# Optimization experiments

Hardware: AMD Instinct MI355X
Metric: run time of the kernel (lower is better)

Reference implementation:

```python
import jax, jax.numpy as jnp
import numpy as np

N_NODES = 50000
N_EDGES = 800000
IN_F = 128
OUT_F = 32
HEADS = 4
EDGE_DIM = 8
ALPHA = 0.2  # LeakyReLU negative slope


def setup_inputs() -> dict:
    key = jax.random.key(0)
    k0, k1, k2, k3, k4 = jax.random.split(key, 5)
    x = jax.random.normal(k0, (N_NODES, IN_F), dtype=jnp.float32)
    edge_index = jax.random.randint(k1, (2, N_EDGES), 0, N_NODES, dtype=jnp.int32)
    edge_attr = jax.random.normal(k2, (N_EDGES, EDGE_DIM), dtype=jnp.float32)
    # xavier-ish init for parameters
    W = jax.random.normal(k3, (HEADS, IN_F, OUT_F), dtype=jnp.float32) * (1.0 / np.float32(np.sqrt(IN_F)))
    a = jax.random.normal(k4, (HEADS, 2 * OUT_F + EDGE_DIM, 1), dtype=jnp.float32) * np.float32(0.1)
    return {"x": x, "edge_index": edge_index, "edge_attr": edge_attr, "W": W, "a": a}


def reference(x, edge_index, edge_attr, W, a):
    n_nodes = x.shape[0]
    out_f = W.shape[2]
    src, dst = edge_index[0], edge_index[1]

    # per-head linear transform: (N, H, O)
    xt = jnp.einsum('ni,hio->nho', x, W)
    x_src = xt[src]  # (E, H, O) edge gather
    x_dst = xt[dst]  # (E, H, O)

    # split attention vector a = [a_src | a_dst | a_edge]; equivalent to
    # einsum('ehi,hio->eho', cat([x_src, x_dst, edge]), a) without the concat
    av = a[..., 0]                      # (H, 2O+D)
    a_s = av[:, :out_f]                 # (H, O)
    a_d = av[:, out_f:2 * out_f]        # (H, O)
    a_e = av[:, 2 * out_f:]             # (H, D)
    e = (jnp.einsum('eho,ho->eh', x_src, a_s)
         + jnp.einsum('eho,ho->eh', x_dst, a_d)
         + edge_attr @ a_e.T)           # (E, H)
    e = jnp.where(e > 0, e, ALPHA * e)  # LeakyReLU

    # segment (per-destination) softmax over incoming edges, per head
    max_e = jax.ops.segment_max(e, dst, num_segments=n_nodes)   # (N, H), -inf on empty
    max_e = jnp.where(jnp.isneginf(max_e), jnp.zeros_like(max_e), max_e)
    exp_e = jnp.exp(e - max_e[dst])                             # (E, H)
    sum_exp = jax.ops.segment_sum(exp_e, dst, num_segments=n_nodes)  # (N, H)
    attention = exp_e / (sum_exp[dst] + 1e-10)                  # (E, H)

    # weighted scatter-add aggregation
    weighted = x_src * attention[:, :, None]                    # (E, H, O)
    out = jax.ops.segment_sum(weighted, dst, num_segments=n_nodes)  # (N, H, O)
    return out.reshape(n_nodes, -1)  # concat=True -> (N, H*O)
```

## Files before the change

### kernel.cpp

```cpp
#include <hip/hip_runtime.h>
#include <hip/hip_fp16.h>

#define N_NODES 50000
#define N_EDGES 800000
#define IN_F    128
#define OUT_F   32
#define HEADS   4
#define EDGE_DIM 8
#define LRELU_ALPHA 0.2f

#define EPB 2048
#define BT  1024
#define EPT (EPB / BT)
#define NBUCK 98
#define NBLK_A ((N_EDGES + EPB - 1) / EPB)
#define NODES_PER_BUCK 512
#define CAP 10240

typedef float    floatx4 __attribute__((ext_vector_type(4)));
typedef unsigned uintx4  __attribute__((ext_vector_type(4)));
typedef short    short4v __attribute__((ext_vector_type(4)));
typedef short    short8v __attribute__((ext_vector_type(8)));
typedef float    f32x4   __attribute__((ext_vector_type(4)));

__device__ __forceinline__ unsigned f2bf(float f) {
  unsigned u = __float_as_uint(f);
  return (u + 0x7fffu + ((u >> 16) & 1u)) >> 16;
}

__global__ __launch_bounds__(128) void k_wprep(
    const float* __restrict__ W, unsigned short* __restrict__ wtg,
    unsigned* __restrict__ bfill) {
  const int row = blockIdx.x;
  const int i = threadIdx.x;
  if (row == 0 && i < NBUCK) bfill[i] = (unsigned)(i * CAP);
  const float v = W[(row >> 5) * (IN_F * OUT_F) + i * OUT_F + (row & 31)];
  wtg[row * 128 + i] = (unsigned short)f2bf(v);
}

__global__ __launch_bounds__(256) void k_transform(
    const float* __restrict__ x, const unsigned short* __restrict__ wtg,
    unsigned* __restrict__ xtb) {
  __shared__ short sxb[64][136];
  const int t = threadIdx.x;
  const int n0 = blockIdx.x * 64;

#pragma unroll
  for (int r = 0; r < 8; ++r) {
    const int f = r * 256 + t;
    const int node = f >> 5;
    const int i4 = (f & 31) * 4;
    const int n = n0 + node;
    float4 v = make_float4(0.f, 0.f, 0.f, 0.f);
    if (n < N_NODES) v = *reinterpret_cast<const float4*>(&x[(size_t)n * 128 + i4]);
    short4v s4;
    s4.x = (short)f2bf(v.x);
    s4.y = (short)f2bf(v.y);
    s4.z = (short)f2bf(v.z);
    s4.w = (short)f2bf(v.w);
    *reinterpret_cast<short4v*>(&sxb[node][i4]) = s4;
  }
  __syncthreads();

  const int w = t >> 6;
  const int lane = t & 63;
  const int r16 = lane & 15;
  const int kg = lane >> 4;

  f32x4 acc[8];
#pragma unroll
  for (int nt = 0; nt < 8; ++nt) acc[nt] = (f32x4)(0.f);

#pragma unroll
  for (int kk = 0; kk < 4; ++kk) {
    const short8v afrag =
        *reinterpret_cast<const short8v*>(&sxb[w * 16 + r16][kk * 32 + kg * 8]);
#pragma unroll
    for (int nt = 0; nt < 8; ++nt) {
      const short8v bfrag = *reinterpret_cast<const short8v*>(
          &wtg[(nt * 16 + r16) * 128 + kk * 32 + kg * 8]);
      acc[nt] = __builtin_amdgcn_mfma_f32_16x16x32_bf16(afrag, bfrag, acc[nt],
                                                        0, 0, 0);
    }
  }

#pragma unroll
  for (int nt = 0; nt < 8; ++nt) {
#pragma unroll
    for (int reg = 0; reg < 4; ++reg) {
      const float v = acc[nt][reg];
      const float vp = __shfl_xor(v, 1, 64);
      if (!(lane & 1)) {
        const int node = n0 + w * 16 + kg * 4 + reg;
        if (node < N_NODES) {
          const unsigned u = f2bf(v) | (f2bf(vp) << 16);
          xtb[(size_t)node * 64 + nt * 8 + (r16 >> 1)] = u;
        }
      }
    }
  }
}

__global__ __launch_bounds__(256) void k_alpha(
    const unsigned* __restrict__ xtb, const float* __restrict__ a,
    float* __restrict__ alpha_src, float* __restrict__ alpha_dst) {
  const int t = threadIdx.x;
  const int node = blockIdx.x * 64 + (t >> 2);
  if (node >= N_NODES) return;
  const int q = t & 3;
  const unsigned* __restrict__ row = &xtb[(size_t)node * 64 + q * 16];
  const float* __restrict__ as = &a[q * 72];
  const float* __restrict__ ad = &a[q * 72 + 32];
  float s = 0.f, d = 0.f;
#pragma unroll
  for (int j = 0; j < 16; ++j) {
    const unsigned u = row[j];
    const float lo = __uint_as_float(u << 16);
    const float hi = __uint_as_float(u & 0xffff0000u);
    s = fmaf(lo, as[2 * j], s);
    s = fmaf(hi, as[2 * j + 1], s);
    d = fmaf(lo, ad[2 * j], d);
    d = fmaf(hi, ad[2 * j + 1], d);
  }
  alpha_src[node * 4 + q] = s;
  alpha_dst[node * 4 + q] = d;
}

__device__ __forceinline__ uintx4 make_entry(
    int e, int src, int dst, const float* __restrict__ ea,
    const float* __restrict__ a, const float* __restrict__ alpha_src,
    const float* __restrict__ alpha_dst) {
  const floatx4 ev0 = __builtin_nontemporal_load(
      reinterpret_cast<const floatx4*>(&ea[(size_t)e * EDGE_DIM]));
  const floatx4 ev1 = __builtin_nontemporal_load(
      reinterpret_cast<const floatx4*>(&ea[(size_t)e * EDGE_DIM + 4]));
  const float4 als = *reinterpret_cast<const float4*>(&alpha_src[src * 4]);
  const float4 ald = *reinterpret_cast<const float4*>(&alpha_dst[dst * 4]);
  const float* alsp = reinterpret_cast<const float*>(&als);
  const float* aldp = reinterpret_cast<const float*>(&ald);
  unsigned sh[4];
#pragma unroll
  for (int h = 0; h < HEADS; ++h) {
    float s = alsp[h] + aldp[h];
    const float* ae = &a[h * 72 + 64];
    s = fmaf(ev0.x, ae[0], s);
    s = fmaf(ev0.y, ae[1], s);
    s = fmaf(ev0.z, ae[2], s);
    s = fmaf(ev0.w, ae[3], s);
    s = fmaf(ev1.x, ae[4], s);
    s = fmaf(ev1.y, ae[5], s);
    s = fmaf(ev1.z, ae[6], s);
    s = fmaf(ev1.w, ae[7], s);
    s = s > 0.f ? s : LRELU_ALPHA * s;
    sh[h] = (unsigned)__half_as_ushort(__float2half(s));
  }
  uintx4 ent;
  ent.x = (unsigned)src;
  ent.y = sh[0] | (sh[1] << 16);
  ent.z = sh[2] | (sh[3] << 16);
  ent.w = (unsigned)dst;
  return ent;
}

__global__ __launch_bounds__(BT) void k_binsort(
    const int* __restrict__ ei, const float* __restrict__ ea,
    const float* __restrict__ a, const float* __restrict__ alpha_src,
    const float* __restrict__ alpha_dst, unsigned* __restrict__ bfill,
    uintx4* __restrict__ stage) {
  __shared__ uintx4 sent[EPB];
  __shared__ unsigned lhist[128];
  __shared__ unsigned lscan[128];
  __shared__ unsigned gb[128];
  const int t = threadIdx.x;
  const int e0 = blockIdx.x * EPB;
  const int nvalid = min(EPB, N_EDGES - e0);

  if (t < 128) lhist[t] = 0u;
  __syncthreads();

  uintx4 ent[EPT];
  int bk[EPT];
  int lpos[EPT];
#pragma unroll
  for (int k = 0; k < EPT; ++k) {
    const int e = e0 + k * BT + t;
    bk[k] = -1;
    if (e < N_EDGES) {
      const int src = __builtin_nontemporal_load(&ei[e]);
      const int dst = __builtin_nontemporal_load(&ei[N_EDGES + e]);
      ent[k] = make_entry(e, src, dst, ea, a, alpha_src, alpha_dst);
      bk[k] = dst >> 9;
      lpos[k] = (int)atomicAdd(&lhist[bk[k]], 1u);
    }
  }
  __syncthreads();

  if (t < 128) lscan[t] = lhist[t];
  __syncthreads();
#pragma unroll
  for (int off = 1; off < 128; off <<= 1) {
    unsigned v = 0u;
    if (t < 128 && t >= off) v = lscan[t - off];
    __syncthreads();
    if (t < 128) lscan[t] += v;
    __syncthreads();
  }
  if (t < NBUCK) {
    const unsigned cnt = lhist[t];
    lscan[t] -= cnt;
    gb[t] = cnt ? atomicAdd(&bfill[t], cnt) : 0u;
  }
  __syncthreads();

#pragma unroll
  for (int k = 0; k < EPT; ++k) {
    if (bk[k] >= 0) {
      const int p = (int)lscan[bk[k]] + lpos[k];
      sent[p] = ent[k];
    }
  }
  __syncthreads();

#pragma unroll
  for (int k = 0; k < EPT; ++k) {
    const int p = k * BT + t;
    if (p < nvalid) {
      const uintx4 sv = sent[p];
      const int b = (int)(sv.w >> 9);
      stage[gb[b] + (unsigned)(p - (int)lscan[b])] = sv;
    }
  }
}

__global__ __launch_bounds__(1024) void k_place(
    const unsigned* __restrict__ bfill, const uintx4* __restrict__ stage,
    unsigned* __restrict__ rs, uintx4* __restrict__ csr) {
  __shared__ unsigned lbuf[NODES_PER_BUCK];
  __shared__ unsigned wsum[8];
  __shared__ unsigned bscan[128];
  const int b = blockIdx.x;
  const int t = threadIdx.x;
  const int node0 = b << 9;
  const int nn = min(NODES_PER_BUCK, N_NODES - node0);
  const unsigned base = (unsigned)(b * CAP);

  if (t < 128) {
    bscan[t] = (t < NBUCK) ? (bfill[t] - (unsigned)(t * CAP)) : 0u;
  }
  __syncthreads();
#pragma unroll
  for (int off = 1; off < 128; off <<= 1) {
    unsigned v = 0u;
    if (t < 128 && t >= off) v = bscan[t - off];
    __syncthreads();
    if (t < 128) bscan[t] += v;
    __syncthreads();
  }
  const unsigned cnt = bfill[b] - base;
  const unsigned bs = (b == 0) ? 0u : bscan[b - 1];

  if (t < NODES_PER_BUCK) lbuf[t] = 0u;
  __syncthreads();

  for (unsigned i = t; i < cnt; i += 1024) {
    const unsigned dst = __builtin_nontemporal_load(&stage[base + i]).w;
    atomicAdd(&lbuf[dst - (unsigned)node0], 1u);
  }
  __syncthreads();

  const unsigned c = (t < NODES_PER_BUCK) ? lbuf[t] : 0u;
  unsigned incl = c;
  const int lane = t & 63;
#pragma unroll
  for (int off = 1; off < 64; off <<= 1) {
    const unsigned n = __shfl_up(incl, off, 64);
    if (lane >= off) incl += n;
  }
  if (t < NODES_PER_BUCK && lane == 63) wsum[t >> 6] = incl;
  __syncthreads();
  if (t < 8) {
    const unsigned wv = wsum[t];
    unsigned wincl = wv;
#pragma unroll
    for (int off = 1; off < 8; off <<= 1) {
      const unsigned n = __shfl_up(wincl, off, 64);
      if (t >= off) wincl += n;
    }
    wsum[t] = wincl - wv;
  }
  __syncthreads();
  if (t < NODES_PER_BUCK) {
    const unsigned excl = incl - c + wsum[t >> 6];
    lbuf[t] = bs + excl;
    if (t < nn) rs[node0 + t] = bs + excl;
  }
  if (b == NBUCK - 1 && t == 0) rs[N_NODES] = N_EDGES;
  __syncthreads();

  for (unsigned i = t; i < cnt; i += 1024) {
    const uintx4 ent = __builtin_nontemporal_load(&stage[base + i]);
    const unsigned slot = atomicAdd(&lbuf[ent.w - (unsigned)node0], 1u);
    csr[slot] = ent;
  }
}

__device__ __forceinline__ float ent_score(const uintx4& ent, int hA) {
  const unsigned uu = (hA < 2) ? ent.y : ent.z;
  const unsigned us = (hA & 1) ? (uu >> 16) : (uu & 0xffffu);
  return __half2float(__ushort_as_half((unsigned short)us));
}

__global__ __launch_bounds__(256) void k_agg(
    const unsigned* __restrict__ rs, const uintx4* __restrict__ csr,
    const unsigned* __restrict__ xtb, float* __restrict__ out) {
  const int lane = threadIdx.x & 63;
  const int dst = (int)((blockIdx.x * (unsigned)blockDim.x + threadIdx.x) >> 6);
  if (dst >= N_NODES) return;

  const unsigned j0 = rs[dst];
  const unsigned j1 = rs[dst + 1];
  const int deg = (int)(j1 - j0);

  float a0 = 0.f, a1 = 0.f, lsum = 0.f;

  if (deg > 0) {
    const int rounds = (deg + 15) >> 4;
    const int sub = lane >> 2;
    const int hA = lane & 3;
    const int hB = lane >> 4;

    const uintx4 pad = {0u, 0xfc00fc00u, 0xfc00fc00u, 0u};

    for (int r = 0; r < rounds; ++r) {
      const int base = (int)j0 + r * 16;
      const int j = base + sub;
      const uintx4 ent =
          (j < (int)j1) ? __builtin_nontemporal_load(&csr[j]) : pad;
      const float w = __expf(ent_score(ent, hA));
      lsum += w;
      const int sx = (int)ent.x;

      int srcs[16];
#pragma unroll
      for (int jj = 0; jj < 16; ++jj) srcs[jj] = __shfl(sx, 4 * jj, 64);
      unsigned ud[16];
#pragma unroll
      for (int jj = 0; jj < 16; ++jj)
        ud[jj] = xtb[(size_t)srcs[jj] * 64 + lane];
#pragma unroll
      for (int jj = 0; jj < 16; ++jj) {
        const float wj = __shfl(w, 4 * jj + hB, 64);
        a0 = fmaf(wj, __uint_as_float(ud[jj] << 16), a0);
        a1 = fmaf(wj, __uint_as_float(ud[jj] & 0xffff0000u), a1);
      }
    }
    lsum += __shfl_xor(lsum, 4, 64);
    lsum += __shfl_xor(lsum, 8, 64);
    lsum += __shfl_xor(lsum, 16, 64);
    lsum += __shfl_xor(lsum, 32, 64);
    lsum = __shfl(lsum, hB, 64);
  }

  const float inv = 1.0f / (lsum + 1e-10f);
  __builtin_nontemporal_store(a0 * inv, &out[(size_t)dst * 128 + lane * 2 + 0]);
  __builtin_nontemporal_store(a1 * inv, &out[(size_t)dst * 128 + lane * 2 + 1]);
}

extern "C" void kernel_launch(void* const* d_in, const int* in_sizes, int n_in,
                              void* d_out, int out_size, void* d_ws,
                              size_t ws_size, hipStream_t stream) {
  const float* x = (const float*)d_in[0];
  const int* ei = (const int*)d_in[1];
  const float* ea = (const float*)d_in[2];
  const float* W = (const float*)d_in[3];
  const float* a = (const float*)d_in[4];
  float* out = (float*)d_out;

  char* p = (char*)d_ws;
  unsigned* xtb = (unsigned*)p;     p += (size_t)N_NODES * 64 * 4;
  uintx4* csr = (uintx4*)p;         p += (size_t)N_EDGES * 16;
  uintx4* stage = (uintx4*)p;       p += (size_t)NBUCK * CAP * 16;
  float* alpha_src = (float*)p;     p += (size_t)N_NODES * 4 * 4;
  float* alpha_dst = (float*)p;     p += (size_t)N_NODES * 4 * 4;
  unsigned* rs = (unsigned*)p;      p += (size_t)(N_NODES + 1) * 4;
  unsigned* bfill = (unsigned*)p;   p += 128 * 4;
  unsigned short* wtg = (unsigned short*)p; p += 128 * 128 * 2;

  k_wprep<<<128, 128, 0, stream>>>(W, wtg, bfill);
  k_transform<<<(N_NODES + 63) / 64, 256, 0, stream>>>(x, wtg, xtb);
  k_alpha<<<(N_NODES + 63) / 64, 256, 0, stream>>>(xtb, a, alpha_src,
                                                   alpha_dst);
  k_binsort<<<NBLK_A, BT, 0, stream>>>(ei, ea, a, alpha_src, alpha_dst, bfill,
                                       stage);
  k_place<<<NBUCK, 1024, 0, stream>>>(bfill, stage, rs, csr);
  k_agg<<<(N_NODES * 64 + 255) / 256, 256, 0, stream>>>(rs, csr, xtb, out);
}
```

Baseline: 122.8 us.

## Restructure node transform to 16-node blocks without shared-memory staging

```diff
diff --git a/kernel.cpp b/kernel.cpp
--- a/kernel.cpp
+++ b/kernel.cpp
@@ -19,7 +19,6 @@
 
 typedef float    floatx4 __attribute__((ext_vector_type(4)));
 typedef unsigned uintx4  __attribute__((ext_vector_type(4)));
-typedef short    short4v __attribute__((ext_vector_type(4)));
 typedef short    short8v __attribute__((ext_vector_type(8)));
 typedef float    f32x4   __attribute__((ext_vector_type(4)));
 
@@ -41,62 +40,48 @@
 __global__ __launch_bounds__(256) void k_transform(
     const float* __restrict__ x, const unsigned short* __restrict__ wtg,
     unsigned* __restrict__ xtb) {
-  __shared__ short sxb[64][136];
   const int t = threadIdx.x;
-  const int n0 = blockIdx.x * 64;
-
-#pragma unroll
-  for (int r = 0; r < 8; ++r) {
-    const int f = r * 256 + t;
-    const int node = f >> 5;
-    const int i4 = (f & 31) * 4;
-    const int n = n0 + node;
-    float4 v = make_float4(0.f, 0.f, 0.f, 0.f);
-    if (n < N_NODES) v = *reinterpret_cast<const float4*>(&x[(size_t)n * 128 + i4]);
-    short4v s4;
-    s4.x = (short)f2bf(v.x);
-    s4.y = (short)f2bf(v.y);
-    s4.z = (short)f2bf(v.z);
-    s4.w = (short)f2bf(v.w);
-    *reinterpret_cast<short4v*>(&sxb[node][i4]) = s4;
-  }
-  __syncthreads();
-
   const int w = t >> 6;
   const int lane = t & 63;
   const int r16 = lane & 15;
   const int kg = lane >> 4;
-
-  f32x4 acc[8];
-#pragma unroll
-  for (int nt = 0; nt < 8; ++nt) acc[nt] = (f32x4)(0.f);
-
-#pragma unroll
+  const int n0 = blockIdx.x * 16;
+  const float* __restrict__ xrow = &x[(size_t)(n0 + r16) * 128];
+
+  f32x4 acc0 = (f32x4)(0.f);
+  f32x4 acc1 = (f32x4)(0.f);
+  const int nt0 = w * 2;
+
+#pragma unroll 1
   for (int kk = 0; kk < 4; ++kk) {
-    const short8v afrag =
-        *reinterpret_cast<const short8v*>(&sxb[w * 16 + r16][kk * 32 + kg * 8]);
-#pragma unroll
-    for (int nt = 0; nt < 8; ++nt) {
-      const short8v bfrag = *reinterpret_cast<const short8v*>(
-          &wtg[(nt * 16 + r16) * 128 + kk * 32 + kg * 8]);
-      acc[nt] = __builtin_amdgcn_mfma_f32_16x16x32_bf16(afrag, bfrag, acc[nt],
-                                                        0, 0, 0);
-    }
-  }
-
-#pragma unroll
-  for (int nt = 0; nt < 8; ++nt) {
-#pragma unroll
-    for (int reg = 0; reg < 4; ++reg) {
-      const float v = acc[nt][reg];
-      const float vp = __shfl_xor(v, 1, 64);
-      if (!(lane & 1)) {
-        const int node = n0 + w * 16 + kg * 4 + reg;
-        if (node < N_NODES) {
-          const unsigned u = f2bf(v) | (f2bf(vp) << 16);
-          xtb[(size_t)node * 64 + nt * 8 + (r16 >> 1)] = u;
-        }
-      }
+    const int koff = kk * 32 + kg * 8;
+    const float4 xa = *reinterpret_cast<const float4*>(&xrow[koff]);
+    const float4 xb = *reinterpret_cast<const float4*>(&xrow[koff + 4]);
+    short8v af;
+    af[0] = (short)f2bf(xa.x); af[1] = (short)f2bf(xa.y);
+    af[2] = (short)f2bf(xa.z); af[3] = (short)f2bf(xa.w);
+    af[4] = (short)f2bf(xb.x); af[5] = (short)f2bf(xb.y);
+    af[6] = (short)f2bf(xb.z); af[7] = (short)f2bf(xb.w);
+    const short8v bf0 = *reinterpret_cast<const short8v*>(
+        &wtg[(nt0 * 16 + r16) * 128 + koff]);
+    const short8v bf1 = *reinterpret_cast<const short8v*>(
+        &wtg[((nt0 + 1) * 16 + r16) * 128 + koff]);
+    acc0 = __builtin_amdgcn_mfma_f32_16x16x32_bf16(af, bf0, acc0, 0, 0, 0);
+    acc1 = __builtin_amdgcn_mfma_f32_16x16x32_bf16(af, bf1, acc1, 0, 0, 0);
+  }
+
+#pragma unroll
+  for (int reg = 0; reg < 4; ++reg) {
+    const int onode = n0 + kg * 4 + reg;
+    const float v0 = acc0[reg];
+    const float p0 = __shfl_xor(v0, 1, 64);
+    const float v1 = acc1[reg];
+    const float p1 = __shfl_xor(v1, 1, 64);
+    if (!(lane & 1)) {
+      xtb[(size_t)onode * 64 + nt0 * 8 + (r16 >> 1)] =
+          f2bf(v0) | (f2bf(p0) << 16);
+      xtb[(size_t)onode * 64 + (nt0 + 1) * 8 + (r16 >> 1)] =
+          f2bf(v1) | (f2bf(p1) << 16);
     }
   }
 }
@@ -387,7 +372,7 @@
   unsigned short* wtg = (unsigned short*)p; p += 128 * 128 * 2;
 
   k_wprep<<<128, 128, 0, stream>>>(W, wtg, bfill);
-  k_transform<<<(N_NODES + 63) / 64, 256, 0, stream>>>(x, wtg, xtb);
+  k_transform<<<N_NODES / 16, 256, 0, stream>>>(x, wtg, xtb);
   k_alpha<<<(N_NODES + 63) / 64, 256, 0, stream>>>(xtb, a, alpha_src,
                                                    alpha_dst);
   k_binsort<<<NBLK_A, BT, 0, stream>>>(ei, ea, a, alpha_src, alpha_dst, bfill,
```

New measurement: 125.8 us. 1.02x slower.
